# Performance work log

Measured on AMD Instinct MI355X. Metric: run time of the kernel, lower is better.

## Reference

```python
import jax, jax.numpy as jnp
import numpy as np
from jax import lax

EPS = 1e-5  # torch BatchNorm default eps

# Binarization with straight-through estimator (hard-tanh gradient window),
# matching BinaryFunc in dizcza/MCMC_BinaryNet.
@jax.custom_vjp
def binarize(x):
    return jnp.sign(x)

def _bin_fwd(x):
    return jnp.sign(x), x

def _bin_bwd(res, g):
    return (g * (jnp.abs(res) <= 1.0).astype(g.dtype),)

binarize.defvjp(_bin_fwd, _bin_bwd)

def bn2d(x, gamma, beta):
    # training-mode BatchNorm2d: batch stats over (N,H,W), biased variance
    m = x.mean(axis=(0, 2, 3), keepdims=True)
    v = x.var(axis=(0, 2, 3), keepdims=True)
    xn = (x - m) * lax.rsqrt(v + EPS)
    return xn * gamma[None, :, None, None] + beta[None, :, None, None]

def bn1d(x, gamma, beta):
    m = x.mean(axis=0, keepdims=True)
    v = x.var(axis=0, keepdims=True)
    return (x - m) * lax.rsqrt(v + EPS) * gamma[None, :] + beta[None, :]

def bconv(x, w):
    # BinaryDecorator(Conv2d): sign(x) conv sign(W), padding=0, no bias
    return lax.conv_general_dilated(binarize(x), binarize(w), (1, 1), 'VALID',
                                    dimension_numbers=('NCHW', 'OIHW', 'NCHW'))

def maxpool2(x):
    return lax.reduce_window(x, -jnp.inf, lax.max, (1, 1, 2, 2), (1, 1, 2, 2), 'VALID')

def prelu(x, a):
    return jnp.where(x >= 0, x, a * x)


def setup_inputs() -> dict:
    key = jax.random.key(0)
    ks = iter(jax.random.split(key, 16))
    conv_channels = [3, 128, 256, 512]
    fc_sizes = [512 * 6 * 6, 1024, 10]
    d = {'x': jax.random.normal(next(ks), (128, 3, 64, 64), jnp.float32)}
    for i, (cin, cout) in enumerate(zip(conv_channels[:-1], conv_channels[1:])):
        d[f'cg{i}'] = jnp.ones((cin,), jnp.float32)          # BN2d gamma
        d[f'cb{i}'] = jnp.zeros((cin,), jnp.float32)         # BN2d beta
        d[f'cw{i}'] = jax.random.normal(next(ks), (cout, cin, 3, 3), jnp.float32) * 0.05
        d[f'cp{i}'] = jnp.full((1,), 0.25, jnp.float32)      # PReLU (num_parameters=1)
    for i, (fin, fout) in enumerate(zip(fc_sizes[:-1], fc_sizes[1:])):
        d[f'fg{i}'] = jnp.ones((fin,), jnp.float32)
        d[f'fb{i}'] = jnp.zeros((fin,), jnp.float32)
        d[f'fw{i}'] = jax.random.normal(next(ks), (fout, fin), jnp.float32) * 0.05
        d[f'fp{i}'] = jnp.full((1,), 0.25, jnp.float32)
    d['scale'] = jnp.full((1,), 1e-3, jnp.float32)           # ScaleLayer init
    return d


def reference(x, cg0, cb0, cw0, cp0, cg1, cb1, cw1, cp1, cg2, cb2, cw2, cp2,
              fg0, fb0, fw0, fp0, fg1, fb1, fw1, fp1, scale):
    for cg, cb, cw, cp in ((cg0, cb0, cw0, cp0), (cg1, cb1, cw1, cp1), (cg2, cb2, cw2, cp2)):
        x = bn2d(x, cg, cb)
        x = bconv(x, cw)
        x = maxpool2(x)
        x = prelu(x, cp)
    x = x.reshape(x.shape[0], -1)  # [B, 512*6*6]
    for fg, fb, fw, fp in ((fg0, fb0, fw0, fp0), (fg1, fb1, fw1, fp1)):
        x = bn1d(x, fg, fb)
        x = binarize(x) @ binarize(fw).T  # BinaryDecorator(Linear), no bias
        x = prelu(x, fp)
    return x * scale
```

## Files before the change

kernel.cpp:

```cpp
#include <hip/hip_runtime.h>
#include <cstdint>
#include <cstddef>

#define BN_EPS 1e-5


__global__ void zero_d(double* p, int n) {
  int i = blockIdx.x * blockDim.x + threadIdx.x;
  if (i < n) p[i] = 0.0;
}

__global__ void reduce_plane(const float* __restrict__ x, double* __restrict__ sums,
                             int C, int HW) {
  int c = blockIdx.x, n = blockIdx.y;
  const float* p = x + ((long)n * C + c) * HW;
  double s = 0.0, s2 = 0.0;
  for (int i = threadIdx.x; i < HW; i += blockDim.x) {
    double v = (double)p[i];
    s += v; s2 += v * v;
  }
  for (int o = 32; o > 0; o >>= 1) {
    s  += __shfl_down(s, o, 64);
    s2 += __shfl_down(s2, o, 64);
  }
  __shared__ double ls[4], ls2[4];
  int lane = threadIdx.x & 63, w = threadIdx.x >> 6;
  if (lane == 0) { ls[w] = s; ls2[w] = s2; }
  __syncthreads();
  if (threadIdx.x == 0) {
    double a = 0, b = 0;
    for (int i = 0; i < 4; i++) { a += ls[i]; b += ls2[i]; }
    atomicAdd(&sums[2 * c], a);
    atomicAdd(&sums[2 * c + 1], b);
  }
}

__global__ void reduce_cl(const float* __restrict__ x, double* __restrict__ sums,
                          int C, long rows) {
  int lane = threadIdx.x & 63, wv = threadIdx.x >> 6;
  int c = blockIdx.x * 64 + lane;
  double s = 0.0, s2 = 0.0;
  for (long r = blockIdx.y * 4 + wv; r < rows; r += (long)gridDim.y * 4) {
    double v = (double)x[r * C + c];
    s += v; s2 += v * v;
  }
  __shared__ double ls[4][64], ls2[4][64];
  ls[wv][lane] = s; ls2[wv][lane] = s2;
  __syncthreads();
  if (threadIdx.x < 64) {
    double a = ls[0][lane] + ls[1][lane] + ls[2][lane] + ls[3][lane];
    double b = ls2[0][lane] + ls2[1][lane] + ls2[2][lane] + ls2[3][lane];
    atomicAdd(&sums[2 * c], a);
    atomicAdd(&sums[2 * c + 1], b);
  }
}

__global__ void reduce_cols2(const float* __restrict__ x, double* __restrict__ sums,
                             int R, int F, int RS) {
  int f = blockIdx.x * blockDim.x + threadIdx.x;
  int r0 = blockIdx.y * RS, r1 = min(r0 + RS, R);
  double s = 0.0, s2 = 0.0;
  for (int r = r0; r < r1; r++) {
    double v = (double)x[(long)r * F + f];
    s += v; s2 += v * v;
  }
  atomicAdd(&sums[2 * f], s);
  atomicAdd(&sums[2 * f + 1], s2);
}

__global__ void finalize_stats(const double* __restrict__ sums, double2* __restrict__ st,
                               int C, double cnt) {
  int c = blockIdx.x * blockDim.x + threadIdx.x;
  if (c >= C) return;
  double m = sums[2 * c] / cnt;
  double v = sums[2 * c + 1] / cnt - m * m;
  st[c] = make_double2(m, 1.0 / sqrt(v + BN_EPS));
}


__global__ void pack_bits_c1(const float* __restrict__ x, const double2* __restrict__ st,
                             const float* __restrict__ g, const float* __restrict__ b,
                             uint64_t* __restrict__ rows) {
  int wid = blockIdx.x * 4 + (threadIdx.x >> 6);
  int lane = threadIdx.x & 63;
  int n = wid / 192, rem = wid % 192;
  int ci = rem >> 6, y = rem & 63;
  double2 s = st[ci];
  float xv = x[(((long)n * 3 + ci) * 64 + y) * 64 + lane];
  float xn = (float)(((double)xv - s.x) * s.y) * g[ci] + b[ci];
  uint64_t m = __ballot(xn > 0.f);
  if (lane == 0) rows[wid] = m;
}

__global__ void pack_wc1(const float* __restrict__ w, uint32_t* __restrict__ wm) {
  int co = threadIdx.x;
  uint32_t m = 0;
  for (int j = 0; j < 27; j++) m |= (uint32_t)(w[co * 27 + j] > 0.f) << j;
  wm[co] = m;
}

__global__ void pack_cl(const float* __restrict__ acl, const double2* __restrict__ st,
                        const float* __restrict__ g, const float* __restrict__ b,
                        uint64_t* __restrict__ out, int C, long nwords, int lw) {
  long wid = (long)blockIdx.x * 4 + (threadIdx.x >> 6);
  if (wid >= nwords) return;
  int lane = threadIdx.x & 63;
  long row = wid >> lw;
  int w = (int)(wid & ((1 << lw) - 1));
  int c = w * 64 + lane;
  double2 s = st[c];
  float xv = acl[row * C + c];
  float xn = (float)(((double)xv - s.x) * s.y) * g[c] + b[c];
  uint64_t m = __ballot(xn > 0.f);
  if (lane == 0) out[wid] = m;
}

__global__ void pack_wconv(const float* __restrict__ w, uint64_t* __restrict__ out,
                           int CO, int CI, int W) {
  int i = blockIdx.x * blockDim.x + threadIdx.x;
  int total = CO * 9 * W;
  if (i >= total) return;
  int wd = i % W;
  int t = i / W;
  int tap = t % 9, co = t / 9;
  uint64_t bits = 0;
  for (int k = 0; k < 64; k++) {
    int ci = wd * 64 + k;
    bits |= (uint64_t)(w[((long)co * CI + ci) * 9 + tap] > 0.f) << k;
  }
  out[i] = bits;
}

__global__ void pack_nz(const float* __restrict__ x, const double2* __restrict__ st,
                        const float* __restrict__ g, const float* __restrict__ b,
                        uint64_t* __restrict__ out, int R, int F) {
  int Wf = F >> 6;
  long wid = (long)blockIdx.x * 4 + (threadIdx.x >> 6);
  if (wid >= (long)R * Wf) return;
  int lane = threadIdx.x & 63;
  long r = wid / Wf;
  int w = (int)(wid % Wf);
  int f = w * 64 + lane;
  double2 s = st[f];
  double d = (double)x[r * F + f] - s.x;
  float xn = (float)(d * s.y) * g[f] + b[f];
  uint64_t sm = __ballot(xn > 0.f);
  uint64_t nm = __ballot(d != 0.0);
  if (lane == 0) { out[2 * wid] = sm; out[2 * wid + 1] = nm; }
}

__global__ void pack_wfc2_t(const float* __restrict__ w, uint64_t* __restrict__ out,
                            int O, int F) {
  int Wf = F >> 6;
  long wid = (long)blockIdx.x * 4 + (threadIdx.x >> 6);
  if (wid >= (long)O * Wf) return;
  int lane = threadIdx.x & 63;
  long o = wid / Wf;
  int wd = (int)(wid % Wf);
  uint64_t m = __ballot(w[o * F + wd * 64 + lane] > 0.f);
  if (lane == 0) out[(long)wd * O + o] = m;
}


__global__ __launch_bounds__(256) void conv1_pool3(const uint64_t* __restrict__ rows,
                                                   const uint32_t* __restrict__ wm,
                                                   const float* __restrict__ cp,
                                                   float* __restrict__ out) {
  __shared__ uint64_t rL[192];
  __shared__ uint32_t wL[128];
  __shared__ uint32_t mL[61 * 4];
  int n = blockIdx.y, chunk = blockIdx.x, t = threadIdx.x;
  if (t < 192) rL[t] = rows[n * 192 + t];
  if (t < 128) wL[t] = wm[t];
  __syncthreads();
  if (t < 244) {
    int pl = t >> 2, quad = t & 3;
    int pos = chunk * 61 + pl;
    if (pos < 961) {
      int py = pos / 31, px = pos - py * 31;
      int cy = 2 * py + (quad >> 1), cx = 2 * px + (quad & 1);
      uint32_t m = 0;
#pragma unroll
      for (int ci = 0; ci < 3; ci++)
#pragma unroll
        for (int ky = 0; ky < 3; ky++)
          m |= (uint32_t)((rL[ci * 64 + cy + ky] >> cx) & 7) << (ci * 9 + ky * 3);
      mL[pl * 4 + quad] = m;
    }
  }
  __syncthreads();
  int co = t & 127, slot = t >> 7;
  float alpha = cp[0];
  uint32_t w = wL[co];
  for (int i = slot; i < 61; i += 2) {
    int pos = chunk * 61 + i;
    if (pos >= 961) break;
    int p0 = __popc(mL[4 * i] ^ w);
    int p1 = __popc(mL[4 * i + 1] ^ w);
    int p2 = __popc(mL[4 * i + 2] ^ w);
    int p3 = __popc(mL[4 * i + 3] ^ w);
    int dot = 27 - 2 * min(min(p0, p1), min(p2, p3));
    float f = (float)dot;
    out[((long)n * 961 + pos) * 128 + co] = dot >= 0 ? f : alpha * f;
  }
}


#define ROW6(aL, aR, x0, x1, x2, x3, wa, wb, wc)                                \
  aL += __popcll((x0) ^ (wa)) + __popcll((x1) ^ (wb)) + __popcll((x2) ^ (wc)); \
  aR += __popcll((x1) ^ (wa)) + __popcll((x2) ^ (wb)) + __popcll((x3) ^ (wc));

#define CSTEP(C00, C01, C10, C11, C20, C21, C30, C31,                     \
              D00, D01, D10, D11, D20, D21, D30, D31)                     \
  {                                                                       \
    D00 = rq[0];   D01 = rq[2];                                           \
    D10 = rq[62];  D11 = rq[64];                                          \
    D20 = rq[124]; D21 = rq[126];                                         \
    D30 = rq[186]; D31 = rq[188];                                         \
    int a00 = 0, a01 = 0, a10 = 0, a11 = 0;                               \
    ROW6(a00, a01, C00, C01, D00, D01, w0, w1, w2)                        \
    ROW6(a00, a01, C10, C11, D10, D11, w3, w4, w5)                        \
    ROW6(a10, a11, C10, C11, D10, D11, w0, w1, w2)                        \
    ROW6(a00, a01, C20, C21, D20, D21, w6, w7, w8)                        \
    ROW6(a10, a11, C20, C21, D20, D21, w3, w4, w5)                        \
    ROW6(a10, a11, C30, C31, D30, D31, w6, w7, w8)                        \
    int t00 = a00 + __shfl_xor(a00, 32);                                  \
    int t01 = a01 + __shfl_xor(a01, 32);                                  \
    int t10 = a10 + __shfl_xor(a10, 32);                                  \
    int t11 = a11 + __shfl_xor(a11, 32);                                  \
    if (h == 0) {                                                         \
      int dot = 1152 - 2 * min(min(t00, t01), min(t10, t11));             \
      float ff = (float)dot;                                              \
      *outp = dot >= 0 ? ff : alpha * ff;                                 \
    }                                                                     \
    rq += 4; outp += 256;                                                 \
  }

__global__ __attribute__((amdgpu_flat_work_group_size(256, 256),
                          amdgpu_waves_per_eu(4, 6)))
void convs2(const uint64_t* __restrict__ in, const uint64_t* __restrict__ wt,
            const float* __restrict__ cp, float* __restrict__ out) {
  __shared__ uint64_t sIn[10 * 31 * 2];
  int n = blockIdx.y;
  int cg = blockIdx.x >> 2, chunk = blockIdx.x & 3;
  int t = threadIdx.x, lane = t & 63, slot = t >> 6;
  int r0 = chunk * 8;
  int nr = min(10, 31 - r0);
  const uint64_t* src = in + ((long)n * 31 + r0) * 62;
  for (int i = t; i < nr * 62; i += 256) sIn[i] = src[i];
  int h = lane >> 5;
  int co = cg * 32 + (lane & 31);
  const uint64_t* wg = wt + co * 18 + h;
  uint64_t w0 = wg[0],  w1 = wg[2],  w2 = wg[4];
  uint64_t w3 = wg[6],  w4 = wg[8],  w5 = wg[10];
  uint64_t w6 = wg[12], w7 = wg[14], w8 = wg[16];
  __syncthreads();
  int py = chunk * 4 + slot;
  if (py >= 14) return;
  float alpha = cp[0];
  const uint64_t* rp = sIn + (2 * slot) * 62 + h;
  uint64_t c00 = rp[0],   c01 = rp[2];
  uint64_t c10 = rp[62],  c11 = rp[64];
  uint64_t c20 = rp[124], c21 = rp[126];
  uint64_t c30 = rp[186], c31 = rp[188];
  uint64_t d00, d01, d10, d11, d20, d21, d30, d31;
  const uint64_t* rq = rp + 4;
  float* outp = out + ((long)n * 196 + py * 14) * 256 + co;
  for (int px2 = 0; px2 < 7; px2++) {
    CSTEP(c00, c01, c10, c11, c20, c21, c30, c31,
          d00, d01, d10, d11, d20, d21, d30, d31)
    CSTEP(d00, d01, d10, d11, d20, d21, d30, d31,
          c00, c01, c10, c11, c20, c21, c30, c31)
  }
}

#define TAP2(acc, P, wa, wb) acc += __popcll((P).x ^ (wa)) + __popcll((P).y ^ (wb));
#define ROWT(aL, aR, pA, pB, pC, pD, WX, WY, WZ)                \
  TAP2(aL, pA, WX.x, WX.y) TAP2(aL, pB, WY.x, WY.y)             \
  TAP2(aL, pC, WZ.x, WZ.y)                                      \
  TAP2(aR, pB, WX.x, WX.y) TAP2(aR, pC, WY.x, WY.y)             \
  TAP2(aR, pD, WZ.x, WZ.y)

__global__ __attribute__((amdgpu_flat_work_group_size(256, 256),
                          amdgpu_waves_per_eu(4, 6)))
void convs3(const uint64_t* __restrict__ in, const uint64_t* __restrict__ wt,
            const float* __restrict__ cp, float* __restrict__ out) {
  __shared__ uint64_t sIn[14 * 14 * 4];
  int n = blockIdx.y, cg = blockIdx.x;
  int t = threadIdx.x, lane = t & 63, slot = t >> 6;
  const uint64_t* src = in + (long)n * 784;
  for (int i = t; i < 784; i += 256) sIn[i] = src[i];
  int h = lane >> 5;
  int co = cg * 32 + (lane & 31);
  const uint64_t* wg = wt + co * 36 + 2 * h;
  ulonglong2 W0 = *(const ulonglong2*)(wg + 0);
  ulonglong2 W1 = *(const ulonglong2*)(wg + 4);
  ulonglong2 W2 = *(const ulonglong2*)(wg + 8);
  ulonglong2 W3 = *(const ulonglong2*)(wg + 12);
  ulonglong2 W4 = *(const ulonglong2*)(wg + 16);
  ulonglong2 W5 = *(const ulonglong2*)(wg + 20);
  ulonglong2 W6 = *(const ulonglong2*)(wg + 24);
  ulonglong2 W7 = *(const ulonglong2*)(wg + 28);
  ulonglong2 W8 = *(const ulonglong2*)(wg + 32);
  __syncthreads();
  float alpha = cp[0];
  float* outb = out + ((long)n * 512 + co) * 36;
#pragma unroll
  for (int k = 0; k < 9; k++) {
    int pos = slot + 4 * k;
    int py = pos / 6, px = pos - py * 6;
    const uint64_t* q = sIn + ((2 * py) * 14 + 2 * px) * 4 + 2 * h;
    int a00 = 0, a01 = 0, a10 = 0, a11 = 0;
    {
      ulonglong2 p0 = *(const ulonglong2*)(q + 0);
      ulonglong2 p1 = *(const ulonglong2*)(q + 4);
      ulonglong2 p2 = *(const ulonglong2*)(q + 8);
      ulonglong2 p3 = *(const ulonglong2*)(q + 12);
      ROWT(a00, a01, p0, p1, p2, p3, W0, W1, W2)
    }
    {
      const uint64_t* q1 = q + 56;
      ulonglong2 p0 = *(const ulonglong2*)(q1 + 0);
      ulonglong2 p1 = *(const ulonglong2*)(q1 + 4);
      ulonglong2 p2 = *(const ulonglong2*)(q1 + 8);
      ulonglong2 p3 = *(const ulonglong2*)(q1 + 12);
      ROWT(a00, a01, p0, p1, p2, p3, W3, W4, W5)
      ROWT(a10, a11, p0, p1, p2, p3, W0, W1, W2)
    }
    {
      const uint64_t* q2 = q + 112;
      ulonglong2 p0 = *(const ulonglong2*)(q2 + 0);
      ulonglong2 p1 = *(const ulonglong2*)(q2 + 4);
      ulonglong2 p2 = *(const ulonglong2*)(q2 + 8);
      ulonglong2 p3 = *(const ulonglong2*)(q2 + 12);
      ROWT(a00, a01, p0, p1, p2, p3, W6, W7, W8)
      ROWT(a10, a11, p0, p1, p2, p3, W3, W4, W5)
    }
    {
      const uint64_t* q3 = q + 168;
      ulonglong2 p0 = *(const ulonglong2*)(q3 + 0);
      ulonglong2 p1 = *(const ulonglong2*)(q3 + 4);
      ulonglong2 p2 = *(const ulonglong2*)(q3 + 8);
      ulonglong2 p3 = *(const ulonglong2*)(q3 + 12);
      ROWT(a10, a11, p0, p1, p2, p3, W6, W7, W8)
    }
    int t00 = a00 + __shfl_xor(a00, 32);
    int t01 = a01 + __shfl_xor(a01, 32);
    int t10 = a10 + __shfl_xor(a10, 32);
    int t11 = a11 + __shfl_xor(a11, 32);
    if (h == 0) {
      int dot = 2304 - 2 * min(min(t00, t01), min(t10, t11));
      float ff = (float)dot;
      outb[pos] = dot >= 0 ? ff : alpha * ff;
    }
  }
}


__global__ void fc_bin2(const uint64_t* __restrict__ xp, const uint64_t* __restrict__ wp_t,
                        const float* __restrict__ cp, float* __restrict__ out,
                        int O, int Wf) {
  __shared__ uint64_t xs[2][288], xz[2][288];
  int r0 = blockIdx.y * 2;
  for (int i = threadIdx.x; i < 2 * Wf; i += blockDim.x) {
    int rr = i / Wf, wd = i - rr * Wf;
    xs[rr][wd] = xp[(((long)(r0 + rr)) * Wf + wd) * 2];
    xz[rr][wd] = xp[(((long)(r0 + rr)) * Wf + wd) * 2 + 1];
  }
  __syncthreads();
  int o = blockIdx.x * blockDim.x + threadIdx.x;
  if (o >= O) return;
  int pc0 = 0, pc1 = 0, nz0 = 0, nz1 = 0;
  for (int wd = 0; wd < Wf; wd++) {
    uint64_t w = wp_t[(long)wd * O + o];
    uint64_t z0 = xz[0][wd], z1 = xz[1][wd];
    pc0 += __popcll((xs[0][wd] ^ w) & z0);
    pc1 += __popcll((xs[1][wd] ^ w) & z1);
    nz0 += __popcll(z0);
    nz1 += __popcll(z1);
  }
  float alpha = cp[0];
  int d0 = nz0 - 2 * pc0, d1 = nz1 - 2 * pc1;
  float f0 = (float)d0, f1 = (float)d1;
  out[(long)r0 * O + o] = d0 >= 0 ? f0 : alpha * f0;
  out[(long)(r0 + 1) * O + o] = d1 >= 0 ? f1 : alpha * f1;
}

__global__ void fc_bin_scale(const uint64_t* __restrict__ xp, const uint64_t* __restrict__ wp_t,
                             const float* __restrict__ cp, const float* __restrict__ scale,
                             float* __restrict__ out, int R, int O, int Wf) {
  int i = blockIdx.x * blockDim.x + threadIdx.x;
  if (i >= R * O) return;
  int o = i % O, r = i / O;
  int pc = 0, nzc = 0;
  for (int wd = 0; wd < Wf; wd++) {
    uint64_t nz = xp[((long)r * Wf + wd) * 2 + 1];
    pc += __popcll((xp[((long)r * Wf + wd) * 2] ^ wp_t[(long)wd * O + o]) & nz);
    nzc += __popcll(nz);
  }
  int dot = nzc - 2 * pc;
  float f = (float)dot;
  float alpha = cp[0];
  f = dot >= 0 ? f : alpha * f;
  out[i] = f * scale[0];
}


extern "C" void kernel_launch(void* const* d_in, const int* in_sizes, int n_in,
                              void* d_out, int out_size, void* d_ws, size_t ws_size,
                              hipStream_t stream) {
  const float* x   = (const float*)d_in[0];
  const float* cg0 = (const float*)d_in[1];
  const float* cb0 = (const float*)d_in[2];
  const float* cw0 = (const float*)d_in[3];
  const float* cp0 = (const float*)d_in[4];
  const float* cg1 = (const float*)d_in[5];
  const float* cb1 = (const float*)d_in[6];
  const float* cw1 = (const float*)d_in[7];
  const float* cp1 = (const float*)d_in[8];
  const float* cg2 = (const float*)d_in[9];
  const float* cb2 = (const float*)d_in[10];
  const float* cw2 = (const float*)d_in[11];
  const float* cp2 = (const float*)d_in[12];
  const float* fg0 = (const float*)d_in[13];
  const float* fb0 = (const float*)d_in[14];
  const float* fw0 = (const float*)d_in[15];
  const float* fp0 = (const float*)d_in[16];
  const float* fg1 = (const float*)d_in[17];
  const float* fb1 = (const float*)d_in[18];
  const float* fw1 = (const float*)d_in[19];
  const float* fp1 = (const float*)d_in[20];
  const float* scl = (const float*)d_in[21];

  char* ws = (char*)d_ws;
  size_t off = 0;
  auto alloc = [&](size_t bytes) {
    size_t r = off;
    off += (bytes + 255) & ~(size_t)255;
    return r;
  };
  const int C0_OFF = 0, C1_OFF = 16, C2_OFF = 160, C3_OFF = 448, C4_OFF = 18944;
  const int NCH = 19968;

  double*   sums  = (double*)(ws + alloc((size_t)NCH * 2 * sizeof(double)));
  double2*  stats = (double2*)(ws + alloc((size_t)NCH * sizeof(double2)));
  uint64_t* rows0 = (uint64_t*)(ws + alloc(128L * 3 * 64 * 8));
  uint32_t* wm1   = (uint32_t*)(ws + alloc(128L * 4));
  float*    a1    = (float*)(ws + alloc(128L * 961 * 128 * 4));
  uint64_t* s1p   = (uint64_t*)(ws + alloc(128L * 961 * 2 * 8));
  uint64_t* w1p   = (uint64_t*)(ws + alloc(256L * 9 * 2 * 8));
  float*    a2    = (float*)(ws + alloc(128L * 196 * 256 * 4));
  uint64_t* s2p   = (uint64_t*)(ws + alloc(128L * 196 * 4 * 8));
  uint64_t* w2p   = (uint64_t*)(ws + alloc(512L * 9 * 4 * 8));
  float*    a3    = (float*)(ws + alloc(128L * 512 * 36 * 4));
  uint64_t* s3p   = (uint64_t*)(ws + alloc(128L * 288 * 2 * 8));
  uint64_t* w3p   = (uint64_t*)(ws + alloc(1024L * 288 * 8));
  float*    f1    = (float*)(ws + alloc(128L * 1024 * 4));
  uint64_t* s4p   = (uint64_t*)(ws + alloc(128L * 16 * 2 * 8));
  uint64_t* w4p   = (uint64_t*)(ws + alloc(10L * 16 * 8));

  const int B = 256;

  zero_d<<<dim3(156), B, 0, stream>>>(sums, NCH * 2);

  reduce_plane<<<dim3(3, 128), B, 0, stream>>>(x, sums + 2 * C0_OFF, 3, 4096);
  finalize_stats<<<1, 64, 0, stream>>>(sums + 2 * C0_OFF, stats + C0_OFF, 3, 524288.0);
  pack_bits_c1<<<dim3(6144), B, 0, stream>>>(x, stats + C0_OFF, cg0, cb0, rows0);
  pack_wc1<<<1, 128, 0, stream>>>(cw0, wm1);
  conv1_pool3<<<dim3(16, 128), B, 0, stream>>>(rows0, wm1, cp0, a1);

  reduce_cl<<<dim3(2, 256), B, 0, stream>>>(a1, sums + 2 * C1_OFF, 128, 123008L);
  finalize_stats<<<1, 128, 0, stream>>>(sums + 2 * C1_OFF, stats + C1_OFF, 128, 123008.0);
  pack_cl<<<dim3(61504), B, 0, stream>>>(a1, stats + C1_OFF, cg1, cb1, s1p, 128, 246016L, 1);
  pack_wconv<<<dim3(18), B, 0, stream>>>(cw1, w1p, 256, 128, 2);
  convs2<<<dim3(32, 128), B, 0, stream>>>(s1p, w1p, cp1, a2);

  reduce_cl<<<dim3(4, 128), B, 0, stream>>>(a2, sums + 2 * C2_OFF, 256, 25088L);
  finalize_stats<<<1, 256, 0, stream>>>(sums + 2 * C2_OFF, stats + C2_OFF, 256, 25088.0);
  pack_cl<<<dim3(25088), B, 0, stream>>>(a2, stats + C2_OFF, cg2, cb2, s2p, 256, 100352L, 2);
  pack_wconv<<<dim3(72), B, 0, stream>>>(cw2, w2p, 512, 256, 4);
  convs3<<<dim3(16, 128), B, 0, stream>>>(s2p, w2p, cp2, a3);

  reduce_cols2<<<dim3(72, 8), B, 0, stream>>>(a3, sums + 2 * C3_OFF, 128, 18432, 16);
  finalize_stats<<<dim3(72), B, 0, stream>>>(sums + 2 * C3_OFF, stats + C3_OFF, 18432, 128.0);
  pack_nz<<<dim3(9216), B, 0, stream>>>(a3, stats + C3_OFF, fg0, fb0, s3p, 128, 18432);
  pack_wfc2_t<<<dim3(73728), B, 0, stream>>>(fw0, w3p, 1024, 18432);
  fc_bin2<<<dim3(4, 64), B, 0, stream>>>(s3p, w3p, fp0, f1, 1024, 288);

  reduce_cols2<<<dim3(4, 8), B, 0, stream>>>(f1, sums + 2 * C4_OFF, 128, 1024, 16);
  finalize_stats<<<dim3(4), B, 0, stream>>>(sums + 2 * C4_OFF, stats + C4_OFF, 1024, 128.0);
  pack_nz<<<dim3(512), B, 0, stream>>>(f1, stats + C4_OFF, fg1, fb1, s4p, 128, 1024);
  pack_wfc2_t<<<dim3(40), B, 0, stream>>>(fw1, w4p, 10, 1024);
  fc_bin_scale<<<dim3(5), B, 0, stream>>>(s4p, w4p, fp1, scl, (float*)d_out, 128, 10, 16);
}
```

Baseline: 551.7 us.

## Template conv2 with full-channel lanes, drop atomics in BN stats, batch pack kernels

Replaces the hand-written convs2 with a templated convp_carry kernel. Each lane now owns one output channel across all 64 lanes and keeps all weight words in registers, so the cross-half shuffle reduction goes away and fewer blocks are launched. BN statistics for the first layers now write per-block partials that a finalize kernel sums, instead of doing double atomics; zeroing is narrowed to the remaining accumulators. The pack kernels process 8 words per wave, which cuts their grid sizes by a factor of eight. The change adds register pressure from the large weight and column arrays and launches one extra finalize pass per stage.

```diff
diff --git a/kernel.cpp b/kernel.cpp
--- a/kernel.cpp
+++ b/kernel.cpp
@@ -10,8 +10,8 @@
   if (i < n) p[i] = 0.0;
 }
 
-__global__ void reduce_plane(const float* __restrict__ x, double* __restrict__ sums,
-                             int C, int HW) {
+__global__ void reduce_plane_p(const float* __restrict__ x, double* __restrict__ pp,
+                               int C, int HW) {
   int c = blockIdx.x, n = blockIdx.y;
   const float* p = x + ((long)n * C + c) * HW;
   double s = 0.0, s2 = 0.0;
@@ -30,17 +30,31 @@
   if (threadIdx.x == 0) {
     double a = 0, b = 0;
     for (int i = 0; i < 4; i++) { a += ls[i]; b += ls2[i]; }
-    atomicAdd(&sums[2 * c], a);
-    atomicAdd(&sums[2 * c + 1], b);
-  }
-}
-
-__global__ void reduce_cl(const float* __restrict__ x, double* __restrict__ sums,
-                          int C, long rows) {
+    long o = ((long)n * C + c) * 2;
+    pp[o] = a; pp[o + 1] = b;
+  }
+}
+
+__global__ void finalize_plane(const double* __restrict__ pp, double2* __restrict__ st,
+                               int C, int N, double cnt) {
+  int c = threadIdx.x;
+  if (c >= C) return;
+  double s = 0.0, s2 = 0.0;
+  for (int n = 0; n < N; n++) {
+    s  += pp[((long)n * C + c) * 2];
+    s2 += pp[((long)n * C + c) * 2 + 1];
+  }
+  double m = s / cnt;
+  double v = s2 / cnt - m * m;
+  st[c] = make_double2(m, 1.0 / sqrt(v + BN_EPS));
+}
+
+__global__ void reduce_cl_p(const float* __restrict__ x, double* __restrict__ part,
+                            int C, long rows) {
   int lane = threadIdx.x & 63, wv = threadIdx.x >> 6;
   int c = blockIdx.x * 64 + lane;
   double s = 0.0, s2 = 0.0;
-  for (long r = blockIdx.y * 4 + wv; r < rows; r += (long)gridDim.y * 4) {
+  for (long r = (long)blockIdx.y * 4 + wv; r < rows; r += (long)gridDim.y * 4) {
     double v = (double)x[r * C + c];
     s += v; s2 += v * v;
   }
@@ -50,9 +64,23 @@
   if (threadIdx.x < 64) {
     double a = ls[0][lane] + ls[1][lane] + ls[2][lane] + ls[3][lane];
     double b = ls2[0][lane] + ls2[1][lane] + ls2[2][lane] + ls2[3][lane];
-    atomicAdd(&sums[2 * c], a);
-    atomicAdd(&sums[2 * c + 1], b);
-  }
+    long o = (long)blockIdx.y * 2 * C + 2 * c;
+    part[o] = a; part[o + 1] = b;
+  }
+}
+
+__global__ void finalize_parts(const double* __restrict__ part, double2* __restrict__ st,
+                               int C, int Y, double cnt) {
+  int c = blockIdx.x * 64 + threadIdx.x;
+  if (c >= C) return;
+  double s = 0.0, s2 = 0.0;
+  for (int y = 0; y < Y; y++) {
+    s  += part[(long)y * 2 * C + 2 * c];
+    s2 += part[(long)y * 2 * C + 2 * c + 1];
+  }
+  double m = s / cnt;
+  double v = s2 / cnt - m * m;
+  st[c] = make_double2(m, 1.0 / sqrt(v + BN_EPS));
 }
 
 __global__ void reduce_cols2(const float* __restrict__ x, double* __restrict__ sums,
@@ -80,16 +108,20 @@
 
 __global__ void pack_bits_c1(const float* __restrict__ x, const double2* __restrict__ st,
                              const float* __restrict__ g, const float* __restrict__ b,
-                             uint64_t* __restrict__ rows) {
-  int wid = blockIdx.x * 4 + (threadIdx.x >> 6);
+                             uint64_t* __restrict__ rows, int nwid) {
+  long base = ((long)blockIdx.x * 4 + (threadIdx.x >> 6)) * 8;
   int lane = threadIdx.x & 63;
-  int n = wid / 192, rem = wid % 192;
-  int ci = rem >> 6, y = rem & 63;
-  double2 s = st[ci];
-  float xv = x[(((long)n * 3 + ci) * 64 + y) * 64 + lane];
-  float xn = (float)(((double)xv - s.x) * s.y) * g[ci] + b[ci];
-  uint64_t m = __ballot(xn > 0.f);
-  if (lane == 0) rows[wid] = m;
+  for (int j = 0; j < 8; j++) {
+    long wid = base + j;
+    if (wid >= nwid) return;
+    int n = (int)(wid / 192), rem = (int)(wid % 192);
+    int ci = rem >> 6, y = rem & 63;
+    double2 s = st[ci];
+    float xv = x[(((long)n * 3 + ci) * 64 + y) * 64 + lane];
+    float xn = (float)(((double)xv - s.x) * s.y) * g[ci] + b[ci];
+    uint64_t m = __ballot(xn > 0.f);
+    if (lane == 0) rows[wid] = m;
+  }
 }
 
 __global__ void pack_wc1(const float* __restrict__ w, uint32_t* __restrict__ wm) {
@@ -102,17 +134,20 @@
 __global__ void pack_cl(const float* __restrict__ acl, const double2* __restrict__ st,
                         const float* __restrict__ g, const float* __restrict__ b,
                         uint64_t* __restrict__ out, int C, long nwords, int lw) {
-  long wid = (long)blockIdx.x * 4 + (threadIdx.x >> 6);
-  if (wid >= nwords) return;
+  long base = ((long)blockIdx.x * 4 + (threadIdx.x >> 6)) * 8;
   int lane = threadIdx.x & 63;
-  long row = wid >> lw;
-  int w = (int)(wid & ((1 << lw) - 1));
-  int c = w * 64 + lane;
-  double2 s = st[c];
-  float xv = acl[row * C + c];
-  float xn = (float)(((double)xv - s.x) * s.y) * g[c] + b[c];
-  uint64_t m = __ballot(xn > 0.f);
-  if (lane == 0) out[wid] = m;
+  for (int j = 0; j < 8; j++) {
+    long wid = base + j;
+    if (wid >= nwords) return;
+    long row = wid >> lw;
+    int w = (int)(wid & ((1 << lw) - 1));
+    int c = w * 64 + lane;
+    double2 s = st[c];
+    float xv = acl[row * C + c];
+    float xn = (float)(((double)xv - s.x) * s.y) * g[c] + b[c];
+    uint64_t m = __ballot(xn > 0.f);
+    if (lane == 0) out[wid] = m;
+  }
 }
 
 __global__ void pack_wconv(const float* __restrict__ w, uint64_t* __restrict__ out,
@@ -135,30 +170,36 @@
                         const float* __restrict__ g, const float* __restrict__ b,
                         uint64_t* __restrict__ out, int R, int F) {
   int Wf = F >> 6;
-  long wid = (long)blockIdx.x * 4 + (threadIdx.x >> 6);
-  if (wid >= (long)R * Wf) return;
+  long base = ((long)blockIdx.x * 4 + (threadIdx.x >> 6)) * 8;
   int lane = threadIdx.x & 63;
-  long r = wid / Wf;
-  int w = (int)(wid % Wf);
-  int f = w * 64 + lane;
-  double2 s = st[f];
-  double d = (double)x[r * F + f] - s.x;
-  float xn = (float)(d * s.y) * g[f] + b[f];
-  uint64_t sm = __ballot(xn > 0.f);
-  uint64_t nm = __ballot(d != 0.0);
-  if (lane == 0) { out[2 * wid] = sm; out[2 * wid + 1] = nm; }
+  for (int j = 0; j < 8; j++) {
+    long wid = base + j;
+    if (wid >= (long)R * Wf) return;
+    long r = wid / Wf;
+    int w = (int)(wid % Wf);
+    int f = w * 64 + lane;
+    double2 s = st[f];
+    double d = (double)x[r * F + f] - s.x;
+    float xn = (float)(d * s.y) * g[f] + b[f];
+    uint64_t sm = __ballot(xn > 0.f);
+    uint64_t nm = __ballot(d != 0.0);
+    if (lane == 0) { out[2 * wid] = sm; out[2 * wid + 1] = nm; }
+  }
 }
 
 __global__ void pack_wfc2_t(const float* __restrict__ w, uint64_t* __restrict__ out,
                             int O, int F) {
   int Wf = F >> 6;
-  long wid = (long)blockIdx.x * 4 + (threadIdx.x >> 6);
-  if (wid >= (long)O * Wf) return;
+  long base = ((long)blockIdx.x * 4 + (threadIdx.x >> 6)) * 8;
   int lane = threadIdx.x & 63;
-  long o = wid / Wf;
-  int wd = (int)(wid % Wf);
-  uint64_t m = __ballot(w[o * F + wd * 64 + lane] > 0.f);
-  if (lane == 0) out[(long)wd * O + o] = m;
+  for (int j = 0; j < 8; j++) {
+    long wid = base + j;
+    if (wid >= (long)O * Wf) return;
+    long o = wid / Wf;
+    int wd = (int)(wid % Wf);
+    uint64_t m = __ballot(w[o * F + wd * 64 + lane] > 0.f);
+    if (lane == 0) out[(long)wd * O + o] = m;
+  }
 }
 
 
@@ -205,72 +246,74 @@
   }
 }
 
-
-#define ROW6(aL, aR, x0, x1, x2, x3, wa, wb, wc)                                \
-  aL += __popcll((x0) ^ (wa)) + __popcll((x1) ^ (wb)) + __popcll((x2) ^ (wc)); \
-  aR += __popcll((x1) ^ (wa)) + __popcll((x2) ^ (wb)) + __popcll((x3) ^ (wc));
-
-#define CSTEP(C00, C01, C10, C11, C20, C21, C30, C31,                     \
-              D00, D01, D10, D11, D20, D21, D30, D31)                     \
-  {                                                                       \
-    D00 = rq[0];   D01 = rq[2];                                           \
-    D10 = rq[62];  D11 = rq[64];                                          \
-    D20 = rq[124]; D21 = rq[126];                                         \
-    D30 = rq[186]; D31 = rq[188];                                         \
-    int a00 = 0, a01 = 0, a10 = 0, a11 = 0;                               \
-    ROW6(a00, a01, C00, C01, D00, D01, w0, w1, w2)                        \
-    ROW6(a00, a01, C10, C11, D10, D11, w3, w4, w5)                        \
-    ROW6(a10, a11, C10, C11, D10, D11, w0, w1, w2)                        \
-    ROW6(a00, a01, C20, C21, D20, D21, w6, w7, w8)                        \
-    ROW6(a10, a11, C20, C21, D20, D21, w3, w4, w5)                        \
-    ROW6(a10, a11, C30, C31, D30, D31, w6, w7, w8)                        \
-    int t00 = a00 + __shfl_xor(a00, 32);                                  \
-    int t01 = a01 + __shfl_xor(a01, 32);                                  \
-    int t10 = a10 + __shfl_xor(a10, 32);                                  \
-    int t11 = a11 + __shfl_xor(a11, 32);                                  \
-    if (h == 0) {                                                         \
-      int dot = 1152 - 2 * min(min(t00, t01), min(t10, t11));             \
-      float ff = (float)dot;                                              \
-      *outp = dot >= 0 ? ff : alpha * ff;                                 \
-    }                                                                     \
-    rq += 4; outp += 256;                                                 \
-  }
-
+template <int W, int IH, int PH, int CHUNK, bool CL>
 __global__ __attribute__((amdgpu_flat_work_group_size(256, 256),
-                          amdgpu_waves_per_eu(4, 6)))
-void convs2(const uint64_t* __restrict__ in, const uint64_t* __restrict__ wt,
-            const float* __restrict__ cp, float* __restrict__ out) {
-  __shared__ uint64_t sIn[10 * 31 * 2];
+                          amdgpu_waves_per_eu(3, 4)))
+void convp_carry(const uint64_t* __restrict__ in, const uint64_t* __restrict__ wt,
+                 const float* __restrict__ cp, float* __restrict__ out, int CO) {
+  __shared__ uint64_t sIn[10 * IH * W];
   int n = blockIdx.y;
-  int cg = blockIdx.x >> 2, chunk = blockIdx.x & 3;
+  int cg = blockIdx.x / CHUNK, chunk = blockIdx.x % CHUNK;
   int t = threadIdx.x, lane = t & 63, slot = t >> 6;
   int r0 = chunk * 8;
-  int nr = min(10, 31 - r0);
-  const uint64_t* src = in + ((long)n * 31 + r0) * 62;
-  for (int i = t; i < nr * 62; i += 256) sIn[i] = src[i];
-  int h = lane >> 5;
-  int co = cg * 32 + (lane & 31);
-  const uint64_t* wg = wt + co * 18 + h;
-  uint64_t w0 = wg[0],  w1 = wg[2],  w2 = wg[4];
-  uint64_t w3 = wg[6],  w4 = wg[8],  w5 = wg[10];
-  uint64_t w6 = wg[12], w7 = wg[14], w8 = wg[16];
+  int nr = min(10, IH - r0);
+  const uint64_t* src = in + ((long)n * IH + r0) * (IH * W);
+  for (int i = t; i < nr * IH * W; i += 256) sIn[i] = src[i];
+  int co = cg * 64 + lane;
+  uint64_t wr[9 * W];
+  const uint64_t* wg = wt + (long)co * (9 * W);
+#pragma unroll
+  for (int i = 0; i < 9 * W; i++) wr[i] = wg[i];
   __syncthreads();
   int py = chunk * 4 + slot;
-  if (py >= 14) return;
+  if (py >= PH) return;
   float alpha = cp[0];
-  const uint64_t* rp = sIn + (2 * slot) * 62 + h;
-  uint64_t c00 = rp[0],   c01 = rp[2];
-  uint64_t c10 = rp[62],  c11 = rp[64];
-  uint64_t c20 = rp[124], c21 = rp[126];
-  uint64_t c30 = rp[186], c31 = rp[188];
-  uint64_t d00, d01, d10, d11, d20, d21, d30, d31;
-  const uint64_t* rq = rp + 4;
-  float* outp = out + ((long)n * 196 + py * 14) * 256 + co;
-  for (int px2 = 0; px2 < 7; px2++) {
-    CSTEP(c00, c01, c10, c11, c20, c21, c30, c31,
-          d00, d01, d10, d11, d20, d21, d30, d31)
-    CSTEP(d00, d01, d10, d11, d20, d21, d30, d31,
-          c00, c01, c10, c11, c20, c21, c30, c31)
+  const int K = 9 * 64 * W;
+  const uint64_t* base = &sIn[(2 * slot) * (IH * W)];
+  uint64_t c[4][2 * W];
+#pragma unroll
+  for (int cy = 0; cy < 4; cy++) {
+    const uint64_t* p = &base[(cy * IH) * W];
+#pragma unroll
+    for (int j = 0; j < 2 * W; j++) c[cy][j] = p[j];
+  }
+#pragma unroll
+  for (int px = 0; px < PH; px++) {
+    int a00 = 0, a01 = 0, a10 = 0, a11 = 0;
+#pragma unroll
+    for (int cy = 0; cy < 4; cy++) {
+      uint64_t f[2 * W];
+      const uint64_t* fp = &base[(cy * IH + 2 * px + 2) * W];
+#pragma unroll
+      for (int j = 0; j < 2 * W; j++) f[j] = fp[j];
+#pragma unroll
+      for (int col = 0; col < 4; col++) {
+#pragma unroll
+        for (int wd = 0; wd < W; wd++) {
+          uint64_t v = (col < 2) ? c[cy][col * W + wd] : f[(col - 2) * W + wd];
+#pragma unroll
+          for (int dy = 0; dy < 2; dy++) {
+            int ky = cy - dy;
+            if (ky < 0 || ky > 2) continue;
+#pragma unroll
+            for (int dx = 0; dx < 2; dx++) {
+              int kx = col - dx;
+              if (kx < 0 || kx > 2) continue;
+              int p = __popcll(v ^ wr[(ky * 3 + kx) * W + wd]);
+              if (dy == 0) { if (dx == 0) a00 += p; else a01 += p; }
+              else         { if (dx == 0) a10 += p; else a11 += p; }
+            }
+          }
+        }
+      }
+#pragma unroll
+      for (int j = 0; j < 2 * W; j++) c[cy][j] = f[j];
+    }
+    int dot = K - 2 * min(min(a00, a01), min(a10, a11));
+    float f = (float)dot;
+    long idx = CL ? (((long)n * PH * PH + py * PH + px) * CO + co)
+                  : (((long)n * CO + co) * PH * PH + (py * PH + px));
+    out[idx] = dot >= 0 ? f : alpha * f;
   }
 }
 
@@ -444,6 +487,8 @@
 
   double*   sums  = (double*)(ws + alloc((size_t)NCH * 2 * sizeof(double)));
   double2*  stats = (double2*)(ws + alloc((size_t)NCH * sizeof(double2)));
+  double*   parts = (double*)(ws + alloc(512L * 512 * sizeof(double)));
+  double*   pplane= (double*)(ws + alloc(128L * 3 * 2 * sizeof(double)));
   uint64_t* rows0 = (uint64_t*)(ws + alloc(128L * 3 * 64 * 8));
   uint32_t* wm1   = (uint32_t*)(ws + alloc(128L * 4));
   float*    a1    = (float*)(ws + alloc(128L * 961 * 128 * 4));
@@ -461,35 +506,35 @@
 
   const int B = 256;
 
-  zero_d<<<dim3(156), B, 0, stream>>>(sums, NCH * 2);
-
-  reduce_plane<<<dim3(3, 128), B, 0, stream>>>(x, sums + 2 * C0_OFF, 3, 4096);
-  finalize_stats<<<1, 64, 0, stream>>>(sums + 2 * C0_OFF, stats + C0_OFF, 3, 524288.0);
-  pack_bits_c1<<<dim3(6144), B, 0, stream>>>(x, stats + C0_OFF, cg0, cb0, rows0);
+  zero_d<<<dim3(153), B, 0, stream>>>(sums + 2 * C3_OFF, (NCH - C3_OFF) * 2);
+
+  reduce_plane_p<<<dim3(3, 128), B, 0, stream>>>(x, pplane, 3, 4096);
+  finalize_plane<<<1, 64, 0, stream>>>(pplane, stats + C0_OFF, 3, 128, 524288.0);
+  pack_bits_c1<<<dim3(768), B, 0, stream>>>(x, stats + C0_OFF, cg0, cb0, rows0, 24576);
   pack_wc1<<<1, 128, 0, stream>>>(cw0, wm1);
   conv1_pool3<<<dim3(16, 128), B, 0, stream>>>(rows0, wm1, cp0, a1);
 
-  reduce_cl<<<dim3(2, 256), B, 0, stream>>>(a1, sums + 2 * C1_OFF, 128, 123008L);
-  finalize_stats<<<1, 128, 0, stream>>>(sums + 2 * C1_OFF, stats + C1_OFF, 128, 123008.0);
-  pack_cl<<<dim3(61504), B, 0, stream>>>(a1, stats + C1_OFF, cg1, cb1, s1p, 128, 246016L, 1);
+  reduce_cl_p<<<dim3(2, 512), B, 0, stream>>>(a1, parts, 128, 123008L);
+  finalize_parts<<<2, 64, 0, stream>>>(parts, stats + C1_OFF, 128, 512, 123008.0);
+  pack_cl<<<dim3(7688), B, 0, stream>>>(a1, stats + C1_OFF, cg1, cb1, s1p, 128, 246016L, 1);
   pack_wconv<<<dim3(18), B, 0, stream>>>(cw1, w1p, 256, 128, 2);
-  convs2<<<dim3(32, 128), B, 0, stream>>>(s1p, w1p, cp1, a2);
-
-  reduce_cl<<<dim3(4, 128), B, 0, stream>>>(a2, sums + 2 * C2_OFF, 256, 25088L);
-  finalize_stats<<<1, 256, 0, stream>>>(sums + 2 * C2_OFF, stats + C2_OFF, 256, 25088.0);
-  pack_cl<<<dim3(25088), B, 0, stream>>>(a2, stats + C2_OFF, cg2, cb2, s2p, 256, 100352L, 2);
+  convp_carry<2, 31, 14, 4, true><<<dim3(16, 128), B, 0, stream>>>(s1p, w1p, cp1, a2, 256);
+
+  reduce_cl_p<<<dim3(4, 256), B, 0, stream>>>(a2, parts, 256, 25088L);
+  finalize_parts<<<4, 64, 0, stream>>>(parts, stats + C2_OFF, 256, 256, 25088.0);
+  pack_cl<<<dim3(3136), B, 0, stream>>>(a2, stats + C2_OFF, cg2, cb2, s2p, 256, 100352L, 2);
   pack_wconv<<<dim3(72), B, 0, stream>>>(cw2, w2p, 512, 256, 4);
   convs3<<<dim3(16, 128), B, 0, stream>>>(s2p, w2p, cp2, a3);
 
   reduce_cols2<<<dim3(72, 8), B, 0, stream>>>(a3, sums + 2 * C3_OFF, 128, 18432, 16);
   finalize_stats<<<dim3(72), B, 0, stream>>>(sums + 2 * C3_OFF, stats + C3_OFF, 18432, 128.0);
-  pack_nz<<<dim3(9216), B, 0, stream>>>(a3, stats + C3_OFF, fg0, fb0, s3p, 128, 18432);
-  pack_wfc2_t<<<dim3(73728), B, 0, stream>>>(fw0, w3p, 1024, 18432);
+  pack_nz<<<dim3(1152), B, 0, stream>>>(a3, stats + C3_OFF, fg0, fb0, s3p, 128, 18432);
+  pack_wfc2_t<<<dim3(9216), B, 0, stream>>>(fw0, w3p, 1024, 18432);
   fc_bin2<<<dim3(4, 64), B, 0, stream>>>(s3p, w3p, fp0, f1, 1024, 288);
 
   reduce_cols2<<<dim3(4, 8), B, 0, stream>>>(f1, sums + 2 * C4_OFF, 128, 1024, 16);
   finalize_stats<<<dim3(4), B, 0, stream>>>(sums + 2 * C4_OFF, stats + C4_OFF, 1024, 128.0);
-  pack_nz<<<dim3(512), B, 0, stream>>>(f1, stats + C4_OFF, fg1, fb1, s4p, 128, 1024);
-  pack_wfc2_t<<<dim3(40), B, 0, stream>>>(fw1, w4p, 10, 1024);
+  pack_nz<<<dim3(64), B, 0, stream>>>(f1, stats + C4_OFF, fg1, fb1, s4p, 128, 1024);
+  pack_wfc2_t<<<dim3(5), B, 0, stream>>>(fw1, w4p, 10, 1024);
   fc_bin_scale<<<dim3(5), B, 0, stream>>>(s4p, w4p, fp1, scl, (float*)d_out, 128, 10, 16);
 }
```

Result: slower. 706.8 us (+28.1%).
